# Performance work log

Hardware: AMD Instinct MI355X
Metric: run time of the kernel (lower is better)

The kernel has to match this reference:

```python
import math
import jax, jax.numpy as jnp
import numpy as np

H, PQ, PV, E, C, S, N = 12, 4, 8, 16, 128, 384, 512


def setup_inputs() -> dict:
    key = jax.random.key(0)
    ks = jax.random.split(key, 16)
    rn = lambda k, shape, scale=1.0: jax.random.normal(k, shape, jnp.float32) * scale
    single = rn(ks[0], (N, S))
    pair = rn(ks[1], (N, N, C))
    R, _ = jnp.linalg.qr(rn(ks[2], (N, 3, 3)))  # proper orthonormal frames
    t = rn(ks[3], (N, 3))
    w = 0.02
    return dict(
        single_representation=single,
        pair_representation=pair,
        rotations=R,
        translations=t,
        Wq=rn(ks[4], (H, S, E), w),
        Wk=rn(ks[5], (H, S, E), w),
        Wv=rn(ks[6], (H, S, E), w),
        Wqp=rn(ks[7], (H, PQ, S, 3), w),
        Wkp=rn(ks[8], (H, PQ, S, 3), w),
        Wvp=rn(ks[9], (H, PV, S, 3), w),
        Wb=rn(ks[10], (H, C), w),
        Wout=rn(ks[11], (H * (C + E + PV * 4), S), w),
        b_out=jnp.zeros((S,), jnp.float32),
        scale_head=jnp.ones((H,), jnp.float32),
    )


def _frame_apply(R, t, pts):
    # R:[N,3,3], t:[N,3], pts:[H,P,N,3] -> R_n @ p + t_n per residue n
    return jnp.einsum('nij,hpnj->hpni', R, pts) + t[None, None, :, :]


def reference(single_representation, pair_representation, rotations, translations,
              Wq, Wk, Wv, Wqp, Wkp, Wvp, Wb, Wout, b_out, scale_head):
    single, pair = single_representation, pair_representation
    n = single.shape[0]

    # --- sequence QK term ---
    q = jnp.einsum('nd,hde->hne', single, Wq)
    k = jnp.einsum('nd,hde->hne', single, Wk)
    w_single = math.sqrt(1.0 / E) * jnp.einsum('hne,hme->hnm', q, k)  # [H,N,N]

    # --- pair bias term ---
    w_pair = jnp.einsum('nmc,hc->hnm', pair, Wb)  # [H,N,N]

    # --- frame (3D point distance) term ---
    qp = jnp.einsum('nd,hpdk->hpnk', single, Wqp)  # [H,PQ,N,3]
    kp = jnp.einsum('nd,hpdk->hpnk', single, Wkp)
    lqp = _frame_apply(rotations, translations, qp)
    lkp = _frame_apply(rotations, translations, kp)
    diff = lqp[:, :, :, None, :] - lkp[:, :, None, :, :]   # [H,PQ,N,N,3]
    sqd = jnp.sum(diff * diff, axis=(1, 4))                 # [H,N,N] (sum over points & xyz)
    w_frame = (-math.sqrt(1.0 / (18 * PQ))) * jax.nn.softplus(scale_head)[:, None, None] * sqd

    w = jax.nn.softmax(w_single + w_pair + w_frame, axis=-1)  # [H,N,N]

    # --- sequence value aggregation ---
    v = jnp.einsum('nd,hde->hne', single, Wv)
    att_single = jnp.einsum('hnm,hme->hne', w, v)             # [H,N,E]
    att_single = jnp.transpose(att_single, (1, 0, 2)).reshape(n, -1)

    # --- pair value aggregation (faithful to source: sums over query index too) ---
    colsum = jnp.sum(w, axis=1)                               # [H,N] = sum_a w[h,a,b]
    att_pair = jnp.einsum('hb,ibc->hic', colsum, pair)        # [H,N,C]
    att_pair = jnp.transpose(att_pair, (1, 0, 2)).reshape(n, -1)

    # --- 3D point value aggregation ---
    vp = jnp.einsum('nd,hpdk->hpnk', single, Wvp)             # [H,PV,N,3]
    lvp = _frame_apply(rotations, translations, vp)
    local_out = jnp.einsum('hnm,hpmk->hpnk', w, lvp)          # [H,PV,N,3]
    Rinv = jnp.swapaxes(rotations, -1, -2)                    # R^T
    tinv = -jnp.einsum('nij,nj->ni', Rinv, translations)      # -R^T t
    global_out = _frame_apply(Rinv, tinv, local_out)          # [H,PV,N,3]
    out_points = jnp.transpose(global_out, (2, 1, 0, 3)).reshape(n, -1)  # [N, PV*H*3]
    out_norm = jnp.linalg.norm(global_out, axis=-1)           # [H,PV,N]
    out_norm = jnp.transpose(out_norm, (2, 1, 0)).reshape(n, -1)         # [N, PV*H]

    att = jnp.concatenate([att_single, att_pair, out_points, out_norm], axis=-1)
    return att @ Wout + b_out
```

## Files before the change

### kernel.cpp

```cpp
#include <hip/hip_runtime.h>
#include <math.h>

#define NRES 512
#define HH 12
#define PQn 4
#define PVn 8
#define En 16
#define Cn 128
#define Sn 384
#define ATT_COLS 2112

#define OFF_Q    0
#define OFF_K    (OFF_Q   + HH*NRES*En)
#define OFF_V    (OFF_K   + HH*NRES*En)
#define OFF_LQP  (OFF_V   + HH*NRES*En)
#define OFF_LKP  (OFF_LQP + HH*NRES*12)
#define OFF_LVP  (OFF_LKP + HH*NRES*12)
#define OFF_CS   (OFF_LVP + HH*NRES*24)
#define OFF_ATT  (OFF_CS  + NRES*HH)
#define OFF_LG   (OFF_ATT + NRES*ATT_COLS)
#define OFF_PART OFF_LG
#define OFF_KC   OFF_ATT
#define OFF_D1   (OFF_KC + NRES*HH*28)
#define OFF_D0   (OFF_D1 + NRES*HH)
#define OFF_QC   (OFF_D0 + NRES*HH)
#define KSPLIT 16
#define KCHUNK (ATT_COLS/KSPLIT)
#define OROWS 8

__global__ __launch_bounds__(256) void ipa_proj(
    const float* __restrict__ single, const float* __restrict__ Rm,
    const float* __restrict__ tr,
    const float* __restrict__ Wq, const float* __restrict__ Wk,
    const float* __restrict__ Wv, const float* __restrict__ Wqp,
    const float* __restrict__ Wkp, const float* __restrict__ Wvp,
    float* __restrict__ ws)
{
  float* q   = ws + OFF_Q;  float* k   = ws + OFF_K;  float* v   = ws + OFF_V;
  float* lqp = ws + OFF_LQP; float* lkp = ws + OFF_LKP; float* lvp = ws + OFF_LVP;
  const int n0 = blockIdx.x * 8;
  const int g  = blockIdx.y;
  const int tid = threadIdx.x;
  __shared__ float sS[8][388];
  __shared__ float sR[8][9];
  __shared__ float sT[8][3];
  #pragma unroll
  for (int i = 0; i < 3; ++i) {
    int idx = i*256 + tid;
    int r = idx / 96, c4 = idx % 96;
    float4 val = *reinterpret_cast<const float4*>(single + (size_t)(n0 + r)*Sn + c4*4);
    *reinterpret_cast<float4*>(&sS[r][c4*4]) = val;
  }
  if (tid < 72)      sR[tid/9][tid%9] = Rm[(size_t)(n0 + tid/9)*9 + tid%9];
  else if (tid < 96) { int r = (tid-72)/3; sT[r][(tid-72)%3] = tr[(size_t)(n0+r)*3 + (tid-72)%3]; }
  __syncthreads();
  #pragma unroll
  for (int i = 0; i < 3; ++i) {
    int item = i*256 + tid;
    int nl = item & 7;
    int ul = item >> 3;
    int u  = g*96 + ul;
    const float* srow = sS[nl];
    if (u < 576) {
      int which = u/192, r = u%192, h = r>>4, e = r&15;
      const float* W = (which==0 ? Wq : which==1 ? Wk : Wv) + (size_t)h*Sn*En + e;
      float acc = 0.f;
      #pragma unroll 8
      for (int d = 0; d < Sn; ++d) acc = fmaf(srow[d], W[(size_t)d*En], acc);
      float* dst = (which==0 ? q : which==1 ? k : v);
      dst[((size_t)h*NRES + (n0+nl))*En + e] = acc;
    } else {
      int u2 = u - 576;
      const float* W; float* dst;
      if (u2 < 48)      { int h=u2>>2,     p=u2&3;      W = Wqp + (size_t)(h*PQn+p)*Sn*3; dst = lqp + ((size_t)h*NRES + (n0+nl))*12 + p*3; }
      else if (u2 < 96) { int h=(u2-48)>>2,p=(u2-48)&3; W = Wkp + (size_t)(h*PQn+p)*Sn*3; dst = lkp + ((size_t)h*NRES + (n0+nl))*12 + p*3; }
      else              { int h=(u2-96)>>3,p=(u2-96)&7; W = Wvp + (size_t)(h*PVn+p)*Sn*3; dst = lvp + ((size_t)h*NRES + (n0+nl))*24 + p*3; }
      float x0=0.f,x1=0.f,x2=0.f;
      #pragma unroll 4
      for (int d = 0; d < Sn; ++d) {
        float sv = srow[d];
        x0 = fmaf(sv, W[d*3+0], x0);
        x1 = fmaf(sv, W[d*3+1], x1);
        x2 = fmaf(sv, W[d*3+2], x2);
      }
      const float* R8 = sR[nl]; const float* T8 = sT[nl];
      dst[0] = R8[0]*x0 + R8[1]*x1 + R8[2]*x2 + T8[0];
      dst[1] = R8[3]*x0 + R8[4]*x1 + R8[5]*x2 + T8[1];
      dst[2] = R8[6]*x0 + R8[7]*x1 + R8[8]*x2 + T8[2];
    }
  }
}

__global__ __launch_bounds__(256) void ipa_pack(
    const float* __restrict__ scale_head, float* __restrict__ ws)
{
  const float* q   = ws + OFF_Q;
  const float* k   = ws + OFF_K;
  const float* lkp = ws + OFF_LKP;
  const float* lqp = ws + OFF_LQP;
  float* kc = ws + OFF_KC;
  float* qc = ws + OFF_QC;
  float* d1 = ws + OFF_D1;
  float* d0 = ws + OFF_D0;
  const int idx = blockIdx.x*256 + threadIdx.x;
  const int h = idx >> 9, m = idx & 511;
  const float gamma = 0.11785113019775793f * log1pf(__expf(scale_head[h]));
  const float* kr  = k   + ((size_t)h*NRES + m)*En;
  const float* qr  = q   + ((size_t)h*NRES + m)*En;
  const float* lkr = lkp + ((size_t)h*NRES + m)*12;
  const float* lqr = lqp + ((size_t)h*NRES + m)*12;
  float* kcr = kc + ((size_t)m*HH + h)*28;
  float* qcr = qc + ((size_t)m*HH + h)*28;
  #pragma unroll
  for (int e = 0; e < En; ++e) { kcr[e] = 0.25f * kr[e]; qcr[e] = qr[e]; }
  float Bm = 0.f, An = 0.f;
  #pragma unroll
  for (int j = 0; j < 12; ++j) {
    float b = lkr[j], a = lqr[j];
    kcr[16+j] = (2.f*gamma)*b;
    qcr[16+j] = a;
    Bm = fmaf(b, b, Bm);
    An = fmaf(a, a, An);
  }
  d1[m*HH + h] = -gamma*Bm;
  d0[m*HH + h] = -gamma*An;
}

__global__ __launch_bounds__(256) void ipa_logits(
    const float* __restrict__ pair, const float* __restrict__ Wb,
    float* __restrict__ ws)
{
  const float* kc = ws + OFF_KC;
  const float* qc = ws + OFF_QC;
  const float* d1 = ws + OFF_D1;
  const float* d0 = ws + OFF_D0;
  float* lg = ws + OFF_LG;

  __shared__ float sWb[HH*Cn];
  __shared__ float sOut[HH*132];
  for (int i = threadIdx.x; i < HH*Cn/4; i += 256)
    reinterpret_cast<float4*>(sWb)[i] = reinterpret_cast<const float4*>(Wb)[i];
  __syncthreads();

  const int n    = blockIdx.x;
  const int tid  = threadIdx.x;
  const int lane = tid & 63;
  const int wave = tid >> 6;
  const int r    = lane >> 2;
  const int cq   = lane & 3;
  const int ml   = wave*16 + r;
  const int m    = blockIdx.y*128 + ml;
  const int m2   = m + 64;

  const float* p1 = pair + ((size_t)n*NRES + m )*Cn + cq*4;
  const float* p2 = pair + ((size_t)n*NRES + m2)*Cn + cq*4;

  float acc1[HH], acc2[HH];
  #pragma unroll
  for (int h = 0; h < HH; ++h) { acc1[h] = 0.f; acc2[h] = 0.f; }

  #pragma unroll
  for (int jg = 0; jg < 8; ++jg) {
    float4 pv = *reinterpret_cast<const float4*>(p1 + jg*16);
    float4 pw = *reinterpret_cast<const float4*>(p2 + jg*16);
    #pragma unroll
    for (int h = 0; h < HH; ++h) {
      const float4 wb = *reinterpret_cast<const float4*>(&sWb[h*Cn + jg*16 + cq*4]);
      acc1[h] += pv.x*wb.x + pv.y*wb.y + pv.z*wb.z + pv.w*wb.w;
      acc2[h] += pw.x*wb.x + pw.y*wb.y + pw.z*wb.z + pw.w*wb.w;
    }
  }
  #pragma unroll
  for (int h = 0; h < HH; ++h) {
    acc1[h] += __shfl_xor(acc1[h], 1);
    acc1[h] += __shfl_xor(acc1[h], 2);
    acc2[h] += __shfl_xor(acc2[h], 1);
    acc2[h] += __shfl_xor(acc2[h], 2);
  }
  float b10, b11, b12, b20, b21, b22;
  if      (cq == 0) { b10=acc1[0]; b11=acc1[1];  b12=acc1[2];
                      b20=acc2[0]; b21=acc2[1];  b22=acc2[2]; }
  else if (cq == 1) { b10=acc1[3]; b11=acc1[4];  b12=acc1[5];
                      b20=acc2[3]; b21=acc2[4];  b22=acc2[5]; }
  else if (cq == 2) { b10=acc1[6]; b11=acc1[7];  b12=acc1[8];
                      b20=acc2[6]; b21=acc2[7];  b22=acc2[8]; }
  else              { b10=acc1[9]; b11=acc1[10]; b12=acc1[11];
                      b20=acc2[9]; b21=acc2[10]; b22=acc2[11]; }

  const int hb = 3*cq;
  const float* kc1 = kc + ((size_t)m *HH + hb)*28;
  const float* kc2 = kc + ((size_t)m2*HH + hb)*28;
  const float* qcn = qc + ((size_t)n *HH + hb)*28;
  const float* d0n = d0 + (size_t)n*HH + hb;
  const float* d11 = d1 + (size_t)m *HH + hb;
  const float* d12 = d1 + (size_t)m2*HH + hb;

  #pragma unroll
  for (int i = 0; i < 3; ++i) {
    float t1 = (i==0 ? b10 : i==1 ? b11 : b12) + d11[i] + d0n[i];
    float t2 = (i==0 ? b20 : i==1 ? b21 : b22) + d12[i] + d0n[i];
    #pragma unroll
    for (int j = 0; j < 7; ++j) {
      float4 qv = *reinterpret_cast<const float4*>(qcn + i*28 + j*4);
      float4 k1 = *reinterpret_cast<const float4*>(kc1 + i*28 + j*4);
      float4 k2 = *reinterpret_cast<const float4*>(kc2 + i*28 + j*4);
      t1 += k1.x*qv.x + k1.y*qv.y + k1.z*qv.z + k1.w*qv.w;
      t2 += k2.x*qv.x + k2.y*qv.y + k2.z*qv.z + k2.w*qv.w;
    }
    sOut[(hb+i)*132 + ml]      = t1;
    sOut[(hb+i)*132 + ml + 64] = t2;
  }
  __syncthreads();
  for (int idx = tid; idx < HH*32; idx += 256) {
    const int h = idx >> 5, q4 = idx & 31;
    float4 o = make_float4(sOut[h*132 + q4*4 + 0], sOut[h*132 + q4*4 + 1],
                           sOut[h*132 + q4*4 + 2], sOut[h*132 + q4*4 + 3]);
    *reinterpret_cast<float4*>(
        lg + ((size_t)h*NRES + n)*NRES + blockIdx.y*128 + q4*4) = o;
  }
}

__global__ __launch_bounds__(256) void ipa_softmax(float* __restrict__ ws)
{
  float* lg = ws + OFF_LG;
  const int row  = blockIdx.x*4 + (threadIdx.x >> 6);
  const int lane = threadIdx.x & 63;
  float4* p = reinterpret_cast<float4*>(lg + (size_t)row*NRES);
  float4 x0 = p[lane];
  float4 x1 = p[64 + lane];
  float mx = fmaxf(fmaxf(fmaxf(x0.x,x0.y),fmaxf(x0.z,x0.w)),
                   fmaxf(fmaxf(x1.x,x1.y),fmaxf(x1.z,x1.w)));
  #pragma unroll
  for (int off = 32; off >= 1; off >>= 1) mx = fmaxf(mx, __shfl_xor(mx, off));
  x0.x = __expf(x0.x-mx); x0.y = __expf(x0.y-mx); x0.z = __expf(x0.z-mx); x0.w = __expf(x0.w-mx);
  x1.x = __expf(x1.x-mx); x1.y = __expf(x1.y-mx); x1.z = __expf(x1.z-mx); x1.w = __expf(x1.w-mx);
  float sum = x0.x+x0.y+x0.z+x0.w + x1.x+x1.y+x1.z+x1.w;
  #pragma unroll
  for (int off = 32; off >= 1; off >>= 1) sum += __shfl_xor(sum, off);
  const float inv = 1.f/sum;
  x0.x*=inv; x0.y*=inv; x0.z*=inv; x0.w*=inv;
  x1.x*=inv; x1.y*=inv; x1.z*=inv; x1.w*=inv;
  p[lane] = x0;
  p[64 + lane] = x1;
}

__global__ __launch_bounds__(256) void ipa_colsum(float* __restrict__ ws)
{
  const float* lg = ws + OFF_LG;
  float* cs = ws + OFF_CS;
  const int h = blockIdx.x, ac = blockIdx.y, tid = threadIdx.x;
  const float* base = lg + (size_t)h*NRES*NRES + (size_t)ac*64*NRES;
  float acc0 = 0.f, acc1 = 0.f;
  #pragma unroll 4
  for (int a = 0; a < 64; ++a) {
    acc0 += base[(size_t)a*NRES + tid];
    acc1 += base[(size_t)a*NRES + tid + 256];
  }
  atomicAdd(&cs[(size_t)tid*HH + h],       acc0);
  atomicAdd(&cs[(size_t)(tid+256)*HH + h], acc1);
}

__global__ __launch_bounds__(256) void ipa_agg(
    const float* __restrict__ Rm, const float* __restrict__ tr,
    float* __restrict__ ws)
{
  const float* v   = ws + OFF_V;
  const float* lvp = ws + OFF_LVP;
  const float* lg  = ws + OFF_LG;
  float* att = ws + OFF_ATT;
  const int row  = blockIdx.x*4 + (threadIdx.x >> 6);
  const int lane = threadIdx.x & 63;
  const int h = row >> 9, n = row & 511;

  float acc[40];
  #pragma unroll
  for (int i = 0; i < 40; ++i) acc[i] = 0.f;

  const float* wrow = lg + (size_t)row*NRES;
  #pragma unroll 2
  for (int j = 0; j < 8; ++j) {
    const int m = j*64 + lane;
    const float wv = wrow[m];
    const float4* v4 = reinterpret_cast<const float4*>(v + ((size_t)h*NRES + m)*En);
    float4 a0=v4[0], a1=v4[1], a2=v4[2], a3=v4[3];
    acc[0]+=wv*a0.x; acc[1]+=wv*a0.y; acc[2]+=wv*a0.z; acc[3]+=wv*a0.w;
    acc[4]+=wv*a1.x; acc[5]+=wv*a1.y; acc[6]+=wv*a1.z; acc[7]+=wv*a1.w;
    acc[8]+=wv*a2.x; acc[9]+=wv*a2.y; acc[10]+=wv*a2.z; acc[11]+=wv*a2.w;
    acc[12]+=wv*a3.x; acc[13]+=wv*a3.y; acc[14]+=wv*a3.z; acc[15]+=wv*a3.w;
    const float4* l4 = reinterpret_cast<const float4*>(lvp + ((size_t)h*NRES + m)*24);
    #pragma unroll
    for (int t = 0; t < 6; ++t) {
      float4 b = l4[t];
      acc[16+4*t+0]+=wv*b.x; acc[16+4*t+1]+=wv*b.y;
      acc[16+4*t+2]+=wv*b.z; acc[16+4*t+3]+=wv*b.w;
    }
  }
  #pragma unroll
  for (int off = 32; off >= 1; off >>= 1) {
    #pragma unroll
    for (int i = 0; i < 40; ++i) acc[i] += __shfl_xor(acc[i], off);
  }
  if (lane == 0) {
    size_t ab = (size_t)n*ATT_COLS;
    float4* as = reinterpret_cast<float4*>(att + ab + h*En);
    as[0] = make_float4(acc[0],acc[1],acc[2],acc[3]);
    as[1] = make_float4(acc[4],acc[5],acc[6],acc[7]);
    as[2] = make_float4(acc[8],acc[9],acc[10],acc[11]);
    as[3] = make_float4(acc[12],acc[13],acc[14],acc[15]);
    const float R0=Rm[n*9+0],R1=Rm[n*9+1],R2=Rm[n*9+2],
                R3=Rm[n*9+3],R4=Rm[n*9+4],R5=Rm[n*9+5],
                R6=Rm[n*9+6],R7=Rm[n*9+7],R8=Rm[n*9+8];
    const float t0=tr[n*3+0], t1=tr[n*3+1], t2=tr[n*3+2];
    #pragma unroll
    for (int pp = 0; pp < 8; ++pp) {
      float d0 = acc[16+3*pp+0]-t0, d1 = acc[16+3*pp+1]-t1, d2 = acc[16+3*pp+2]-t2;
      float g0 = R0*d0 + R3*d1 + R6*d2;
      float g1 = R1*d0 + R4*d1 + R7*d2;
      float g2 = R2*d0 + R5*d1 + R8*d2;
      att[ab + 1728 + (pp*HH + h)*3 + 0] = g0;
      att[ab + 1728 + (pp*HH + h)*3 + 1] = g1;
      att[ab + 1728 + (pp*HH + h)*3 + 2] = g2;
      att[ab + 2016 + pp*HH + h] = sqrtf(g0*g0 + g1*g1 + g2*g2);
    }
  }
}

__global__ __launch_bounds__(256) void ipa_pairagg(
    const float* __restrict__ pair, float* __restrict__ ws)
{
  const float* cs = ws + OFF_CS;
  float* att = ws + OFF_ATT;
  const int i = blockIdx.x, tid = threadIdx.x;
  __shared__ float sCS[NRES*HH];
  __shared__ float4 sRed[4][HH][32];
  #pragma unroll
  for (int it = 0; it < 6; ++it) {
    int idx = it*256 + tid;
    reinterpret_cast<float4*>(sCS)[idx] = reinterpret_cast<const float4*>(cs)[idx];
  }
  __syncthreads();
  const int c4 = tid & 31, bg = tid >> 5;
  const int b0 = bg * 64;
  float4 acc[HH];
  #pragma unroll
  for (int h = 0; h < HH; ++h) acc[h] = make_float4(0.f,0.f,0.f,0.f);
  const float* prow = pair + (size_t)i*NRES*Cn;
  for (int jb = 0; jb < 64; jb += 4) {
    float4 pv[4];
    #pragma unroll
    for (int u = 0; u < 4; ++u)
      pv[u] = *reinterpret_cast<const float4*>(prow + (size_t)(b0+jb+u)*Cn + c4*4);
    #pragma unroll
    for (int u = 0; u < 4; ++u) {
      const float4* csr = reinterpret_cast<const float4*>(&sCS[(b0+jb+u)*HH]);
      float4 c0 = csr[0], c1 = csr[1], c2 = csr[2];
      float w[12] = {c0.x,c0.y,c0.z,c0.w, c1.x,c1.y,c1.z,c1.w, c2.x,c2.y,c2.z,c2.w};
      #pragma unroll
      for (int h = 0; h < HH; ++h) {
        acc[h].x = fmaf(w[h], pv[u].x, acc[h].x);
        acc[h].y = fmaf(w[h], pv[u].y, acc[h].y);
        acc[h].z = fmaf(w[h], pv[u].z, acc[h].z);
        acc[h].w = fmaf(w[h], pv[u].w, acc[h].w);
      }
    }
  }
  if (bg >= 4) {
    for (int h = 0; h < HH; ++h) sRed[bg-4][h][c4] = acc[h];
  }
  __syncthreads();
  if (bg < 4) {
    for (int h = 0; h < HH; ++h) {
      float4 b2 = sRed[bg][h][c4];
      acc[h].x+=b2.x; acc[h].y+=b2.y; acc[h].z+=b2.z; acc[h].w+=b2.w;
    }
  }
  __syncthreads();
  if (bg >= 2 && bg < 4) {
    for (int h = 0; h < HH; ++h) sRed[bg-2][h][c4] = acc[h];
  }
  __syncthreads();
  if (bg < 2) {
    for (int h = 0; h < HH; ++h) {
      float4 b2 = sRed[bg][h][c4];
      acc[h].x+=b2.x; acc[h].y+=b2.y; acc[h].z+=b2.z; acc[h].w+=b2.w;
    }
  }
  __syncthreads();
  if (bg == 1) {
    for (int h = 0; h < HH; ++h) sRed[0][h][c4] = acc[h];
  }
  __syncthreads();
  if (bg == 0) {
    size_t base = (size_t)i*ATT_COLS + 192;
    for (int h = 0; h < HH; ++h) {
      float4 b2 = sRed[0][h][c4];
      acc[h].x+=b2.x; acc[h].y+=b2.y; acc[h].z+=b2.z; acc[h].w+=b2.w;
      *reinterpret_cast<float4*>(att + base + h*Cn + c4*4) = acc[h];
    }
  }
}

__global__ __launch_bounds__(384) void ipa_outp(
    const float* __restrict__ att, const float* __restrict__ Wout,
    float* __restrict__ ws)
{
  float* partial = ws + OFF_PART;
  const int rb = blockIdx.x;
  const int ks = blockIdx.y;
  const int s  = threadIdx.x;
  const int n0 = rb*OROWS;
  const int j0 = ks*KCHUNK;

  float acc[OROWS];
  #pragma unroll
  for (int r = 0; r < OROWS; ++r) acc[r] = 0.f;

  for (int jg = 0; jg < KCHUNK/4; ++jg) {
    const int j = j0 + jg*4;
    float w0 = Wout[(size_t)(j+0)*Sn + s];
    float w1 = Wout[(size_t)(j+1)*Sn + s];
    float w2 = Wout[(size_t)(j+2)*Sn + s];
    float w3 = Wout[(size_t)(j+3)*Sn + s];
    #pragma unroll
    for (int r = 0; r < OROWS; ++r) {
      float4 av = *reinterpret_cast<const float4*>(att + (size_t)(n0+r)*ATT_COLS + j);
      acc[r] = fmaf(av.x, w0, acc[r]);
      acc[r] = fmaf(av.y, w1, acc[r]);
      acc[r] = fmaf(av.z, w2, acc[r]);
      acc[r] = fmaf(av.w, w3, acc[r]);
    }
  }
  #pragma unroll
  for (int r = 0; r < OROWS; ++r)
    partial[((size_t)ks*NRES + n0 + r)*Sn + s] = acc[r];
}

__global__ __launch_bounds__(384) void ipa_outred(
    const float* __restrict__ b_out, float* __restrict__ ws,
    float* __restrict__ out)
{
  const float* partial = ws + OFF_PART;
  const int n = blockIdx.x, s = threadIdx.x;
  float a = b_out[s];
  #pragma unroll
  for (int ks = 0; ks < KSPLIT; ++ks)
    a += partial[((size_t)ks*NRES + n)*Sn + s];
  out[(size_t)n*Sn + s] = a;
}

extern "C" void kernel_launch(void* const* d_in, const int* in_sizes, int n_in,
                              void* d_out, int out_size, void* d_ws, size_t ws_size,
                              hipStream_t stream) {
  const float* single = (const float*)d_in[0];
  const float* pair   = (const float*)d_in[1];
  const float* Rm     = (const float*)d_in[2];
  const float* tr     = (const float*)d_in[3];
  const float* Wq     = (const float*)d_in[4];
  const float* Wk     = (const float*)d_in[5];
  const float* Wv     = (const float*)d_in[6];
  const float* Wqp    = (const float*)d_in[7];
  const float* Wkp    = (const float*)d_in[8];
  const float* Wvp    = (const float*)d_in[9];
  const float* Wb     = (const float*)d_in[10];
  const float* Wout   = (const float*)d_in[11];
  const float* b_out  = (const float*)d_in[12];
  const float* scale_head = (const float*)d_in[13];
  float* ws  = (float*)d_ws;
  float* out = (float*)d_out;

  hipMemsetAsync(ws + OFF_CS, 0, NRES*HH*sizeof(float), stream);
  ipa_proj   <<<dim3(64, 8),  256, 0, stream>>>(single, Rm, tr, Wq, Wk, Wv, Wqp, Wkp, Wvp, ws);
  ipa_pack   <<<dim3(24),     256, 0, stream>>>(scale_head, ws);
  ipa_logits <<<dim3(NRES, 4), 256, 0, stream>>>(pair, Wb, ws);
  ipa_softmax<<<dim3(HH*NRES/4), 256, 0, stream>>>(ws);
  ipa_colsum <<<dim3(HH, 8),  256, 0, stream>>>(ws);
  ipa_agg    <<<dim3(HH*NRES/4), 256, 0, stream>>>(Rm, tr, ws);
  ipa_pairagg<<<dim3(NRES),   256, 0, stream>>>(pair, ws);
  ipa_outp   <<<dim3(NRES/OROWS, KSPLIT), 384, 0, stream>>>(ws + OFF_ATT, Wout, ws);
  ipa_outred <<<dim3(NRES),   384, 0, stream>>>(b_out, ws, out);
}
```

Measured before the change: 270.6 us.

## Fuse softmax with value aggregation and halve rows per logits block

Merges the softmax and attention-aggregation kernels so normalized weights stay in registers and are consumed directly, avoiding a reread of the logits matrix and one launch. The logits kernel now computes 64 rows per block instead of 128, doubling the grid to raise parallelism, at the cost of reloading Wb into shared memory more often. The fused kernel's column mapping changes to 4 consecutive columns per lane, which alters how the v and lvp loads coalesce. Colsum now runs after the fused kernel and still reads the normalized weights it writes back.

```diff
diff --git a/kernel.cpp b/kernel.cpp
--- a/kernel.cpp
+++ b/kernel.cpp
@@ -137,7 +137,7 @@
   float* lg = ws + OFF_LG;
 
   __shared__ float sWb[HH*Cn];
-  __shared__ float sOut[HH*132];
+  __shared__ float sOut[HH*68];
   for (int i = threadIdx.x; i < HH*Cn/4; i += 256)
     reinterpret_cast<float4*>(sWb)[i] = reinterpret_cast<const float4*>(Wb)[i];
   __syncthreads();
@@ -149,82 +149,73 @@
   const int r    = lane >> 2;
   const int cq   = lane & 3;
   const int ml   = wave*16 + r;
-  const int m    = blockIdx.y*128 + ml;
-  const int m2   = m + 64;
-
-  const float* p1 = pair + ((size_t)n*NRES + m )*Cn + cq*4;
-  const float* p2 = pair + ((size_t)n*NRES + m2)*Cn + cq*4;
-
-  float acc1[HH], acc2[HH];
-  #pragma unroll
-  for (int h = 0; h < HH; ++h) { acc1[h] = 0.f; acc2[h] = 0.f; }
+  const int m    = blockIdx.y*64 + ml;
+
+  const float* p1 = pair + ((size_t)n*NRES + m)*Cn + cq*4;
+
+  float acc[HH];
+  #pragma unroll
+  for (int h = 0; h < HH; ++h) acc[h] = 0.f;
 
   #pragma unroll
   for (int jg = 0; jg < 8; ++jg) {
     float4 pv = *reinterpret_cast<const float4*>(p1 + jg*16);
-    float4 pw = *reinterpret_cast<const float4*>(p2 + jg*16);
     #pragma unroll
     for (int h = 0; h < HH; ++h) {
       const float4 wb = *reinterpret_cast<const float4*>(&sWb[h*Cn + jg*16 + cq*4]);
-      acc1[h] += pv.x*wb.x + pv.y*wb.y + pv.z*wb.z + pv.w*wb.w;
-      acc2[h] += pw.x*wb.x + pw.y*wb.y + pw.z*wb.z + pw.w*wb.w;
+      acc[h] += pv.x*wb.x + pv.y*wb.y + pv.z*wb.z + pv.w*wb.w;
     }
   }
   #pragma unroll
   for (int h = 0; h < HH; ++h) {
-    acc1[h] += __shfl_xor(acc1[h], 1);
-    acc1[h] += __shfl_xor(acc1[h], 2);
-    acc2[h] += __shfl_xor(acc2[h], 1);
-    acc2[h] += __shfl_xor(acc2[h], 2);
-  }
-  float b10, b11, b12, b20, b21, b22;
-  if      (cq == 0) { b10=acc1[0]; b11=acc1[1];  b12=acc1[2];
-                      b20=acc2[0]; b21=acc2[1];  b22=acc2[2]; }
-  else if (cq == 1) { b10=acc1[3]; b11=acc1[4];  b12=acc1[5];
-                      b20=acc2[3]; b21=acc2[4];  b22=acc2[5]; }
-  else if (cq == 2) { b10=acc1[6]; b11=acc1[7];  b12=acc1[8];
-                      b20=acc2[6]; b21=acc2[7];  b22=acc2[8]; }
-  else              { b10=acc1[9]; b11=acc1[10]; b12=acc1[11];
-                      b20=acc2[9]; b21=acc2[10]; b22=acc2[11]; }
+    acc[h] += __shfl_xor(acc[h], 1);
+    acc[h] += __shfl_xor(acc[h], 2);
+  }
+  float b0, b1, b2;
+  if      (cq == 0) { b0=acc[0]; b1=acc[1];  b2=acc[2];  }
+  else if (cq == 1) { b0=acc[3]; b1=acc[4];  b2=acc[5];  }
+  else if (cq == 2) { b0=acc[6]; b1=acc[7];  b2=acc[8];  }
+  else              { b0=acc[9]; b1=acc[10]; b2=acc[11]; }
 
   const int hb = 3*cq;
-  const float* kc1 = kc + ((size_t)m *HH + hb)*28;
-  const float* kc2 = kc + ((size_t)m2*HH + hb)*28;
-  const float* qcn = qc + ((size_t)n *HH + hb)*28;
+  const float* kc1 = kc + ((size_t)m*HH + hb)*28;
+  const float* qcn = qc + ((size_t)n*HH + hb)*28;
   const float* d0n = d0 + (size_t)n*HH + hb;
-  const float* d11 = d1 + (size_t)m *HH + hb;
-  const float* d12 = d1 + (size_t)m2*HH + hb;
+  const float* d11 = d1 + (size_t)m*HH + hb;
 
   #pragma unroll
   for (int i = 0; i < 3; ++i) {
-    float t1 = (i==0 ? b10 : i==1 ? b11 : b12) + d11[i] + d0n[i];
-    float t2 = (i==0 ? b20 : i==1 ? b21 : b22) + d12[i] + d0n[i];
+    float t = (i==0 ? b0 : i==1 ? b1 : b2) + d11[i] + d0n[i];
     #pragma unroll
     for (int j = 0; j < 7; ++j) {
       float4 qv = *reinterpret_cast<const float4*>(qcn + i*28 + j*4);
       float4 k1 = *reinterpret_cast<const float4*>(kc1 + i*28 + j*4);
-      float4 k2 = *reinterpret_cast<const float4*>(kc2 + i*28 + j*4);
-      t1 += k1.x*qv.x + k1.y*qv.y + k1.z*qv.z + k1.w*qv.w;
-      t2 += k2.x*qv.x + k2.y*qv.y + k2.z*qv.z + k2.w*qv.w;
-    }
-    sOut[(hb+i)*132 + ml]      = t1;
-    sOut[(hb+i)*132 + ml + 64] = t2;
-  }
-  __syncthreads();
-  for (int idx = tid; idx < HH*32; idx += 256) {
-    const int h = idx >> 5, q4 = idx & 31;
-    float4 o = make_float4(sOut[h*132 + q4*4 + 0], sOut[h*132 + q4*4 + 1],
-                           sOut[h*132 + q4*4 + 2], sOut[h*132 + q4*4 + 3]);
+      t += k1.x*qv.x + k1.y*qv.y + k1.z*qv.z + k1.w*qv.w;
+    }
+    sOut[(hb+i)*68 + ml] = t;
+  }
+  __syncthreads();
+  if (tid < HH*16) {
+    const int h = tid >> 4, q4 = tid & 15;
+    float4 o = make_float4(sOut[h*68 + q4*4 + 0], sOut[h*68 + q4*4 + 1],
+                           sOut[h*68 + q4*4 + 2], sOut[h*68 + q4*4 + 3]);
     *reinterpret_cast<float4*>(
-        lg + ((size_t)h*NRES + n)*NRES + blockIdx.y*128 + q4*4) = o;
-  }
-}
-
-__global__ __launch_bounds__(256) void ipa_softmax(float* __restrict__ ws)
-{
-  float* lg = ws + OFF_LG;
+        lg + ((size_t)h*NRES + n)*NRES + blockIdx.y*64 + q4*4) = o;
+  }
+}
+
+__global__ __launch_bounds__(256) void ipa_smagg(
+    const float* __restrict__ Rm, const float* __restrict__ tr,
+    float* __restrict__ ws)
+{
+  const float* v   = ws + OFF_V;
+  const float* lvp = ws + OFF_LVP;
+  float* lg  = ws + OFF_LG;
+  float* att = ws + OFF_ATT;
   const int row  = blockIdx.x*4 + (threadIdx.x >> 6);
   const int lane = threadIdx.x & 63;
+  const int h = row >> 9, n = row & 511;
+
   float4* p = reinterpret_cast<float4*>(lg + (size_t)row*NRES);
   float4 x0 = p[lane];
   float4 x1 = p[64 + lane];
@@ -242,57 +233,27 @@
   x1.x*=inv; x1.y*=inv; x1.z*=inv; x1.w*=inv;
   p[lane] = x0;
   p[64 + lane] = x1;
-}
-
-__global__ __launch_bounds__(256) void ipa_colsum(float* __restrict__ ws)
-{
-  const float* lg = ws + OFF_LG;
-  float* cs = ws + OFF_CS;
-  const int h = blockIdx.x, ac = blockIdx.y, tid = threadIdx.x;
-  const float* base = lg + (size_t)h*NRES*NRES + (size_t)ac*64*NRES;
-  float acc0 = 0.f, acc1 = 0.f;
-  #pragma unroll 4
-  for (int a = 0; a < 64; ++a) {
-    acc0 += base[(size_t)a*NRES + tid];
-    acc1 += base[(size_t)a*NRES + tid + 256];
-  }
-  atomicAdd(&cs[(size_t)tid*HH + h],       acc0);
-  atomicAdd(&cs[(size_t)(tid+256)*HH + h], acc1);
-}
-
-__global__ __launch_bounds__(256) void ipa_agg(
-    const float* __restrict__ Rm, const float* __restrict__ tr,
-    float* __restrict__ ws)
-{
-  const float* v   = ws + OFF_V;
-  const float* lvp = ws + OFF_LVP;
-  const float* lg  = ws + OFF_LG;
-  float* att = ws + OFF_ATT;
-  const int row  = blockIdx.x*4 + (threadIdx.x >> 6);
-  const int lane = threadIdx.x & 63;
-  const int h = row >> 9, n = row & 511;
-
+
+  float wv[8] = {x0.x, x0.y, x0.z, x0.w, x1.x, x1.y, x1.z, x1.w};
   float acc[40];
   #pragma unroll
   for (int i = 0; i < 40; ++i) acc[i] = 0.f;
-
-  const float* wrow = lg + (size_t)row*NRES;
-  #pragma unroll 2
-  for (int j = 0; j < 8; ++j) {
-    const int m = j*64 + lane;
-    const float wv = wrow[m];
-    const float4* v4 = reinterpret_cast<const float4*>(v + ((size_t)h*NRES + m)*En);
+  #pragma unroll
+  for (int jj = 0; jj < 8; ++jj) {
+    const int col = (jj < 4) ? (4*lane + jj) : (256 + 4*lane + (jj-4));
+    const float w = wv[jj];
+    const float4* v4 = reinterpret_cast<const float4*>(v + ((size_t)h*NRES + col)*En);
     float4 a0=v4[0], a1=v4[1], a2=v4[2], a3=v4[3];
-    acc[0]+=wv*a0.x; acc[1]+=wv*a0.y; acc[2]+=wv*a0.z; acc[3]+=wv*a0.w;
-    acc[4]+=wv*a1.x; acc[5]+=wv*a1.y; acc[6]+=wv*a1.z; acc[7]+=wv*a1.w;
-    acc[8]+=wv*a2.x; acc[9]+=wv*a2.y; acc[10]+=wv*a2.z; acc[11]+=wv*a2.w;
-    acc[12]+=wv*a3.x; acc[13]+=wv*a3.y; acc[14]+=wv*a3.z; acc[15]+=wv*a3.w;
-    const float4* l4 = reinterpret_cast<const float4*>(lvp + ((size_t)h*NRES + m)*24);
+    acc[0]+=w*a0.x; acc[1]+=w*a0.y; acc[2]+=w*a0.z; acc[3]+=w*a0.w;
+    acc[4]+=w*a1.x; acc[5]+=w*a1.y; acc[6]+=w*a1.z; acc[7]+=w*a1.w;
+    acc[8]+=w*a2.x; acc[9]+=w*a2.y; acc[10]+=w*a2.z; acc[11]+=w*a2.w;
+    acc[12]+=w*a3.x; acc[13]+=w*a3.y; acc[14]+=w*a3.z; acc[15]+=w*a3.w;
+    const float4* l4 = reinterpret_cast<const float4*>(lvp + ((size_t)h*NRES + col)*24);
     #pragma unroll
     for (int t = 0; t < 6; ++t) {
       float4 b = l4[t];
-      acc[16+4*t+0]+=wv*b.x; acc[16+4*t+1]+=wv*b.y;
-      acc[16+4*t+2]+=wv*b.z; acc[16+4*t+3]+=wv*b.w;
+      acc[16+4*t+0]+=w*b.x; acc[16+4*t+1]+=w*b.y;
+      acc[16+4*t+2]+=w*b.z; acc[16+4*t+3]+=w*b.w;
     }
   }
   #pragma unroll
@@ -323,6 +284,22 @@
       att[ab + 2016 + pp*HH + h] = sqrtf(g0*g0 + g1*g1 + g2*g2);
     }
   }
+}
+
+__global__ __launch_bounds__(256) void ipa_colsum(float* __restrict__ ws)
+{
+  const float* lg = ws + OFF_LG;
+  float* cs = ws + OFF_CS;
+  const int h = blockIdx.x, ac = blockIdx.y, tid = threadIdx.x;
+  const float* base = lg + (size_t)h*NRES*NRES + (size_t)ac*64*NRES;
+  float acc0 = 0.f, acc1 = 0.f;
+  #pragma unroll 4
+  for (int a = 0; a < 64; ++a) {
+    acc0 += base[(size_t)a*NRES + tid];
+    acc1 += base[(size_t)a*NRES + tid + 256];
+  }
+  atomicAdd(&cs[(size_t)tid*HH + h],       acc0);
+  atomicAdd(&cs[(size_t)(tid+256)*HH + h], acc1);
 }
 
 __global__ __launch_bounds__(256) void ipa_pairagg(
@@ -471,10 +448,9 @@
   hipMemsetAsync(ws + OFF_CS, 0, NRES*HH*sizeof(float), stream);
   ipa_proj   <<<dim3(64, 8),  256, 0, stream>>>(single, Rm, tr, Wq, Wk, Wv, Wqp, Wkp, Wvp, ws);
   ipa_pack   <<<dim3(24),     256, 0, stream>>>(scale_head, ws);
-  ipa_logits <<<dim3(NRES, 4), 256, 0, stream>>>(pair, Wb, ws);
-  ipa_softmax<<<dim3(HH*NRES/4), 256, 0, stream>>>(ws);
+  ipa_logits <<<dim3(NRES, 8), 256, 0, stream>>>(pair, Wb, ws);
+  ipa_smagg  <<<dim3(HH*NRES/4), 256, 0, stream>>>(Rm, tr, ws);
   ipa_colsum <<<dim3(HH, 8),  256, 0, stream>>>(ws);
-  ipa_agg    <<<dim3(HH*NRES/4), 256, 0, stream>>>(Rm, tr, ws);
   ipa_pairagg<<<dim3(NRES),   256, 0, stream>>>(pair, ws);
   ipa_outp   <<<dim3(NRES/OROWS, KSPLIT), 384, 0, stream>>>(ws + OFF_ATT, Wout, ws);
   ipa_outred <<<dim3(NRES),   384, 0, stream>>>(b_out, ws, out);
```

Result: slower. 296.3 us (+9.5%).
